# Kernel tuning notes

Measured on AMD Instinct MI355X. Metric: run time of the kernel, lower is better.

The kernel has to match this reference:

```python
import jax, jax.numpy as jnp
import numpy as np

HID = (128, 256, 128)  # nmp_qc NNet hidden layer sizes
D_IN = 256
TARGET = 256


def _mlp_params(key, n_in, n_out, prefix):
    sizes = (n_in,) + HID + (n_out,)
    params = {}
    for i in range(len(sizes) - 1):
        key, k1, k2 = jax.random.split(key, 3)
        fan_in = sizes[i]
        bound = 1.0 / np.sqrt(fan_in)
        params[f"{prefix}_W{i}"] = jax.random.uniform(k1, (sizes[i], sizes[i + 1]), jnp.float32, -bound, bound)
        params[f"{prefix}_b{i}"] = jax.random.uniform(k2, (sizes[i + 1],), jnp.float32, -bound, bound)
    return params, key


def _mlp(x, Ws, bs):
    # ReLU on all layers except the last (linear output), matching NNet
    for i in range(len(Ws) - 1):
        x = jax.nn.relu(x @ Ws[i] + bs[i])
    return x @ Ws[-1] + bs[-1]


def setup_inputs() -> dict:
    key = jax.random.key(0)
    k0, k1, key = jax.random.split(key, 3)
    B, N = 512, 256
    inp = {
        "h0": jax.random.normal(k0, (B, N, D_IN), jnp.float32),
        "hT": jax.random.normal(k1, (B, N, D_IN), jnp.float32),
    }
    gp, key = _mlp_params(key, 2 * D_IN, TARGET, "g")  # gate MLP: concat(h0,hT) -> target
    op, key = _mlp_params(key, D_IN, TARGET, "o")      # value MLP: hT -> target
    inp.update(gp)
    inp.update(op)
    return inp


def reference(h0, hT,
              g_W0, g_b0, g_W1, g_b1, g_W2, g_b2, g_W3, g_b3,
              o_W0, o_b0, o_W1, o_b1, o_W2, o_b2, o_W3, o_b3):
    gWs = (g_W0, g_W1, g_W2, g_W3)
    gbs = (g_b0, g_b1, g_b2, g_b3)
    oWs = (o_W0, o_W1, o_W2, o_W3)
    obs = (o_b0, o_b1, o_b2, o_b3)
    # gate: sigmoid(MLP1([h0; hT])) ; value: MLP2(hT)  -- all [B, N, target]
    gate = jax.nn.sigmoid(_mlp(jnp.concatenate([h0, hT], axis=-1), gWs, gbs))
    val = _mlp(hT, oWs, obs)
    # node validity mask: sum of initial features > 0, matching r_mpnn
    mask = (jnp.sum(h0, axis=-1, keepdims=True) > 0).astype(h0.dtype)  # [B, N, 1]
    return jnp.sum(mask * gate * val, axis=1)  # [B, target]
```

## Files before the change

kernel.cpp:

```cpp
#include <hip/hip_runtime.h>
#include <hip/hip_bf16.h>
#include <stdint.h>


typedef __attribute__((ext_vector_type(8))) short short8_t;
typedef __attribute__((ext_vector_type(16))) float f32x16;

#define ROWS 32
#define NWG  4096
#define NTHR 64

#define OFF_X 0
#define OFF_Y 8704
#define OFF_Z 17408
#define OFF_M 22016
#define LDS_TOTAL 22144

__device__ __forceinline__ short f2bf(float f) {
  union { float f; uint32_t u; } v; v.f = f;
  uint32_t r = (v.u + 0x7FFFu + ((v.u >> 16) & 1u)) >> 16;
  return (short)r;
}

template <int KT16, int KSTEPS, int CT>
__device__ __forceinline__ void gemmW(const short* actin, int Sin,
                                      const short* __restrict__ wsB, int ks0, int cb0,
                                      f32x16 (&acc)[CT], int lane) {
  const int n32 = lane & 31, q32 = lane >> 5;
#pragma unroll
  for (int ks = 0; ks < KSTEPS; ++ks) {
    const int kl = ks * 16 + q32 * 8;
    short8_t b[CT];
#pragma unroll
    for (int ct = 0; ct < CT; ++ct)
      b[ct] = *(const short8_t*)(wsB + (((cb0 + ct) * KT16 + ks0 + ks) << 9) + lane * 8);
    const short8_t a = *(const short8_t*)(actin + n32 * Sin + kl);
#pragma unroll
    for (int ct = 0; ct < CT; ++ct)
      acc[ct] = __builtin_amdgcn_mfma_f32_32x32x16_bf16(a, b[ct], acc[ct], 0, 0, 0);
  }
}

template <int CT, int ACTF>
__device__ __forceinline__ void epiW(f32x16 (&acc)[CT], short* actout, int Sout,
                                     const float* __restrict__ bias, int c0,
                                     int n32, int q32) {
#pragma unroll
  for (int ct = 0; ct < CT; ++ct) {
    const int c = c0 + ct * 32 + n32;
    const float bv = bias[c0 + ct * 32 + n32];
#pragma unroll
    for (int reg = 0; reg < 16; ++reg) {
      const int r = (reg & 3) + 8 * (reg >> 2) + 4 * q32;
      float v = acc[ct][reg] + bv;
      if (ACTF == 1) v = fmaxf(v, 0.f);
      actout[r * Sout + c] = f2bf(v);
    }
  }
}

template <bool MASKA>
__device__ __forceinline__ void stage_chunk(const float* __restrict__ src, int row0,
                                            int colbase, short* X, float* maskacc,
                                            int mmode, int lane) {
  const int c4 = lane & 31, rh = lane >> 5;
  float4 v[16];
#pragma unroll
  for (int it = 0; it < 16; ++it)
    v[it] = *(const float4*)(src + (size_t)(row0 + 2 * it + rh) * 256 + colbase + c4 * 4);
#pragma unroll
  for (int it = 0; it < 16; ++it) {
    const int r = 2 * it + rh;
    short4 pk; pk.x = f2bf(v[it].x); pk.y = f2bf(v[it].y); pk.z = f2bf(v[it].z); pk.w = f2bf(v[it].w);
    *(short4*)(X + r * 136 + c4 * 4) = pk;
    if (MASKA && mmode) {
      float s = v[it].x + v[it].y + v[it].z + v[it].w;
      s += __shfl_down(s, 16, 32);
      s += __shfl_down(s, 8, 32);
      s += __shfl_down(s, 4, 32);
      s += __shfl_down(s, 2, 32);
      s += __shfl_down(s, 1, 32);
      if (c4 == 0) {
        if (mmode == 1) maskacc[r] = s; else maskacc[r] += s;
      }
    }
  }
}

template <int NCH, bool MASKA>
__device__ __forceinline__ void streamW(const float* __restrict__ src0,
                                        const float* __restrict__ src1, int splitc,
                                        const short* __restrict__ wsB,
                                        const float* __restrict__ bias,
                                        short* X, short* Aout, float* maskacc,
                                        int row0, int lane) {
  constexpr int KT16 = NCH * 8;
  const int n32 = lane & 31, q32 = lane >> 5;
  f32x16 acc[4];
#pragma unroll
  for (int ct = 0; ct < 4; ++ct) acc[ct] = (f32x16)(0.f);
#pragma unroll
  for (int kc = 0; kc < NCH; ++kc) {
    const bool lo = (kc < splitc);
    const float* src = lo ? src0 : src1;
    const int colbase = (lo ? kc : kc - splitc) * 128;
    const int mm = MASKA ? (kc == 0 ? 1 : (lo ? 2 : 0)) : 0;
    stage_chunk<MASKA>(src, row0, colbase, X, maskacc, mm, lane);
    gemmW<KT16, 8, 4>(X, 136, wsB, kc * 8, 0, acc, lane);
  }
  epiW<4, 1>(acc, Aout, 136, bias, 0, n32, q32);
}

__device__ __forceinline__ void mid_pair(short* A, short* Z,
                                         const short* __restrict__ ws1,
                                         const float* __restrict__ b1,
                                         const short* __restrict__ ws2,
                                         const float* __restrict__ b2,
                                         int lane) {
  const int n32 = lane & 31, q32 = lane >> 5;
  f32x16 acc2[4];
#pragma unroll
  for (int ct = 0; ct < 4; ++ct) acc2[ct] = (f32x16)(0.f);
#pragma unroll
  for (int q = 0; q < 4; ++q) {
    f32x16 acc1[2];
    acc1[0] = (f32x16)(0.f); acc1[1] = (f32x16)(0.f);
    gemmW<8, 8, 2>(A, 136, ws1, 0, q * 2, acc1, lane);
    epiW<2, 1>(acc1, Z, 72, b1 + q * 64, 0, n32, q32);
    gemmW<16, 4, 4>(Z, 72, ws2, q * 4, 0, acc2, lane);
  }
  epiW<4, 1>(acc2, A, 136, b2, 0, n32, q32);
}

__device__ __forceinline__ void final_fuse(const short* Ag, const short* Av,
                                           const short* __restrict__ wsg,
                                           const float* __restrict__ bg,
                                           const short* __restrict__ wsv,
                                           const float* __restrict__ bv,
                                           const float* maskacc, float* __restrict__ out,
                                           int bidx, int lane) {
  const int n32 = lane & 31, q32 = lane >> 5;
#pragma unroll
  for (int q = 0; q < 4; ++q) {
    f32x16 ag[2]; ag[0] = (f32x16)(0.f); ag[1] = (f32x16)(0.f);
    gemmW<8, 8, 2>(Ag, 136, wsg, 0, q * 2, ag, lane);
    f32x16 av[2]; av[0] = (f32x16)(0.f); av[1] = (f32x16)(0.f);
    gemmW<8, 8, 2>(Av, 136, wsv, 0, q * 2, av, lane);
#pragma unroll
    for (int ct = 0; ct < 2; ++ct) {
      const int c = q * 64 + ct * 32 + n32;
      const float gb = bg[c], ob = bv[c];
      float s = 0.f;
#pragma unroll
      for (int reg = 0; reg < 16; ++reg) {
        const int r = (reg & 3) + 8 * (reg >> 2) + 4 * q32;
        if (maskacc[r] > 0.f) {
          const float g = 1.f / (1.f + __expf(-(ag[ct][reg] + gb)));
          s += g * (av[ct][reg] + ob);
        }
      }
      s += __shfl_down(s, 32);
      if (lane < 32) atomicAdd(out + bidx * 256 + c, s);
    }
  }
}

__global__ __launch_bounds__(NTHR, 2)
void readout_main(const float* __restrict__ h0, const float* __restrict__ hT,
                  const short* __restrict__ ws,
                  const float* __restrict__ gb0, const float* __restrict__ gb1,
                  const float* __restrict__ gb2, const float* __restrict__ gb3,
                  const float* __restrict__ ob0, const float* __restrict__ ob1,
                  const float* __restrict__ ob2, const float* __restrict__ ob3,
                  float* __restrict__ out) {
  __shared__ __align__(16) char smem[LDS_TOTAL];
  short* X = (short*)(smem + OFF_X);
  short* Y = (short*)(smem + OFF_Y);
  short* Z = (short*)(smem + OFF_Z);
  float* maskacc = (float*)(smem + OFF_M);

  const int lane = threadIdx.x;
  const int row0 = blockIdx.x * ROWS;
  const int bidx = row0 >> 8;

  streamW<4, true>(h0, hT, 2, ws + 0, gb0, X, Y, maskacc, row0, lane);
  mid_pair(Y, Z, ws + 65536, gb1, ws + 98304, gb2, lane);
  streamW<2, false>(hT, hT, 2, ws + 163840, ob0, X, X, maskacc, row0, lane);
  mid_pair(X, Z, ws + 196608, ob1, ws + 229376, ob2, lane);
  final_fuse(Y, X, ws + 131072, gb3, ws + 262144, ob3, maskacc, out, bidx, lane);
}

__global__ void prep(const float* __restrict__ W0, const float* __restrict__ W1,
                     const float* __restrict__ W2, const float* __restrict__ W3,
                     const float* __restrict__ W4, const float* __restrict__ W5,
                     const float* __restrict__ W6, const float* __restrict__ W7,
                     short* __restrict__ ws, float* __restrict__ out) {
  const int l = blockIdx.y;
  const int le = blockIdx.x * 256 + threadIdx.x;
  if (l == 1) { out[le] = 0.f; out[le + 65536] = 0.f; }
  int K, N, off; const float* W;
  switch (l) {
    case 0:  K = 512; N = 128; off = 0;      W = W0; break;
    case 1:  K = 128; N = 256; off = 65536;  W = W1; break;
    case 2:  K = 256; N = 128; off = 98304;  W = W2; break;
    case 3:  K = 128; N = 256; off = 131072; W = W3; break;
    case 4:  K = 256; N = 128; off = 163840; W = W4; break;
    case 5:  K = 128; N = 256; off = 196608; W = W5; break;
    case 6:  K = 256; N = 128; off = 229376; W = W6; break;
    default: K = 128; N = 256; off = 262144; W = W7; break;
  }
  if (le >= K * N) return;
  const int j = le & 7;
  const int lanei = (le >> 3) & 63;
  const int blk = le >> 9;
  const int kt16 = K >> 4;
  const int ks = blk % kt16, cb = blk / kt16;
  const int n = cb * 32 + (lanei & 31);
  const int k = ks * 16 + (lanei >> 5) * 8 + j;
  ws[off + le] = f2bf(W[k * N + n]);
}

extern "C" void kernel_launch(void* const* d_in, const int* in_sizes, int n_in,
                              void* d_out, int out_size, void* d_ws, size_t ws_size,
                              hipStream_t stream) {
  const float* h0  = (const float*)d_in[0];
  const float* hT  = (const float*)d_in[1];
  const float* gW0 = (const float*)d_in[2];  const float* gb0 = (const float*)d_in[3];
  const float* gW1 = (const float*)d_in[4];  const float* gb1 = (const float*)d_in[5];
  const float* gW2 = (const float*)d_in[6];  const float* gb2 = (const float*)d_in[7];
  const float* gW3 = (const float*)d_in[8];  const float* gb3 = (const float*)d_in[9];
  const float* oW0 = (const float*)d_in[10]; const float* ob0 = (const float*)d_in[11];
  const float* oW1 = (const float*)d_in[12]; const float* ob1 = (const float*)d_in[13];
  const float* oW2 = (const float*)d_in[14]; const float* ob2 = (const float*)d_in[15];
  const float* oW3 = (const float*)d_in[16]; const float* ob3 = (const float*)d_in[17];
  float* out = (float*)d_out;
  short* ws  = (short*)d_ws;

  prep<<<dim3(256, 8), 256, 0, stream>>>(gW0, gW1, gW2, gW3, oW0, oW1, oW2, oW3, ws, out);
  readout_main<<<NWG, NTHR, 0, stream>>>(h0, hT, ws,
                                         gb0, gb1, gb2, gb3,
                                         ob0, ob1, ob2, ob3, out);
}
```

Baseline: 523.9 us.

## Keep gate activations in registers to shrink LDS and raise occupancy

The gate branch's final hidden activations are now held in VGPRs as MFMA A-fragments rather than in a separate LDS buffer Y, so both branches reuse one activation buffer X. The LDS row stride is narrowed from 136 to 132, the staging loads are split into two batches of eight to reduce live registers, and launch bounds now request 3 waves per SIMD. The aim is more resident workgroups to hide global-load latency. The cost is 32 extra VGPRs held across the whole value branch, which may cause spills under the tighter register budget, and the new stride changes the LDS bank-conflict pattern.

```diff
diff --git a/kernel.cpp b/kernel.cpp
--- a/kernel.cpp
+++ b/kernel.cpp
@@ -10,11 +10,13 @@
 #define NWG  4096
 #define NTHR 64
 
+#define SA 132
+#define SZ 72
+
 #define OFF_X 0
-#define OFF_Y 8704
-#define OFF_Z 17408
-#define OFF_M 22016
-#define LDS_TOTAL 22144
+#define OFF_Z 8448
+#define OFF_M 13056
+#define LDS_TOTAL 13184
 
 __device__ __forceinline__ short f2bf(float f) {
   union { float f; uint32_t u; } v; v.f = f;
@@ -41,6 +43,22 @@
   }
 }
 
+template <int KT16, int CT>
+__device__ __forceinline__ void gemmRA(const short8_t (&aR)[8],
+                                       const short* __restrict__ wsB, int cb0,
+                                       f32x16 (&acc)[CT], int lane) {
+#pragma unroll
+  for (int ks = 0; ks < 8; ++ks) {
+    short8_t b[CT];
+#pragma unroll
+    for (int ct = 0; ct < CT; ++ct)
+      b[ct] = *(const short8_t*)(wsB + (((cb0 + ct) * KT16 + ks) << 9) + lane * 8);
+#pragma unroll
+    for (int ct = 0; ct < CT; ++ct)
+      acc[ct] = __builtin_amdgcn_mfma_f32_32x32x16_bf16(aR[ks], b[ct], acc[ct], 0, 0, 0);
+  }
+}
+
 template <int CT, int ACTF>
 __device__ __forceinline__ void epiW(f32x16 (&acc)[CT], short* actout, int Sout,
                                      const float* __restrict__ bias, int c0,
@@ -48,7 +66,7 @@
 #pragma unroll
   for (int ct = 0; ct < CT; ++ct) {
     const int c = c0 + ct * 32 + n32;
-    const float bv = bias[c0 + ct * 32 + n32];
+    const float bv = bias[c];
 #pragma unroll
     for (int reg = 0; reg < 16; ++reg) {
       const int r = (reg & 3) + 8 * (reg >> 2) + 4 * q32;
@@ -64,24 +82,27 @@
                                             int colbase, short* X, float* maskacc,
                                             int mmode, int lane) {
   const int c4 = lane & 31, rh = lane >> 5;
-  float4 v[16];
-#pragma unroll
-  for (int it = 0; it < 16; ++it)
-    v[it] = *(const float4*)(src + (size_t)(row0 + 2 * it + rh) * 256 + colbase + c4 * 4);
-#pragma unroll
-  for (int it = 0; it < 16; ++it) {
-    const int r = 2 * it + rh;
-    short4 pk; pk.x = f2bf(v[it].x); pk.y = f2bf(v[it].y); pk.z = f2bf(v[it].z); pk.w = f2bf(v[it].w);
-    *(short4*)(X + r * 136 + c4 * 4) = pk;
-    if (MASKA && mmode) {
-      float s = v[it].x + v[it].y + v[it].z + v[it].w;
-      s += __shfl_down(s, 16, 32);
-      s += __shfl_down(s, 8, 32);
-      s += __shfl_down(s, 4, 32);
-      s += __shfl_down(s, 2, 32);
-      s += __shfl_down(s, 1, 32);
-      if (c4 == 0) {
-        if (mmode == 1) maskacc[r] = s; else maskacc[r] += s;
+#pragma unroll
+  for (int g = 0; g < 2; ++g) {
+    float4 v[8];
+#pragma unroll
+    for (int it = 0; it < 8; ++it)
+      v[it] = *(const float4*)(src + (size_t)(row0 + g * 16 + 2 * it + rh) * 256 + colbase + c4 * 4);
+#pragma unroll
+    for (int it = 0; it < 8; ++it) {
+      const int r = g * 16 + 2 * it + rh;
+      short4 pk; pk.x = f2bf(v[it].x); pk.y = f2bf(v[it].y); pk.z = f2bf(v[it].z); pk.w = f2bf(v[it].w);
+      *(short4*)(X + r * SA + c4 * 4) = pk;
+      if (MASKA && mmode) {
+        float s = v[it].x + v[it].y + v[it].z + v[it].w;
+        s += __shfl_down(s, 16, 32);
+        s += __shfl_down(s, 8, 32);
+        s += __shfl_down(s, 4, 32);
+        s += __shfl_down(s, 2, 32);
+        s += __shfl_down(s, 1, 32);
+        if (c4 == 0) {
+          if (mmode == 1) maskacc[r] = s; else maskacc[r] += s;
+        }
       }
     }
   }
@@ -92,7 +113,7 @@
                                         const float* __restrict__ src1, int splitc,
                                         const short* __restrict__ wsB,
                                         const float* __restrict__ bias,
-                                        short* X, short* Aout, float* maskacc,
+                                        short* X, float* maskacc,
                                         int row0, int lane) {
   constexpr int KT16 = NCH * 8;
   const int n32 = lane & 31, q32 = lane >> 5;
@@ -106,9 +127,9 @@
     const int colbase = (lo ? kc : kc - splitc) * 128;
     const int mm = MASKA ? (kc == 0 ? 1 : (lo ? 2 : 0)) : 0;
     stage_chunk<MASKA>(src, row0, colbase, X, maskacc, mm, lane);
-    gemmW<KT16, 8, 4>(X, 136, wsB, kc * 8, 0, acc, lane);
-  }
-  epiW<4, 1>(acc, Aout, 136, bias, 0, n32, q32);
+    gemmW<KT16, 8, 4>(X, SA, wsB, kc * 8, 0, acc, lane);
+  }
+  epiW<4, 1>(acc, X, SA, bias, 0, n32, q32);
 }
 
 __device__ __forceinline__ void mid_pair(short* A, short* Z,
@@ -125,14 +146,14 @@
   for (int q = 0; q < 4; ++q) {
     f32x16 acc1[2];
     acc1[0] = (f32x16)(0.f); acc1[1] = (f32x16)(0.f);
-    gemmW<8, 8, 2>(A, 136, ws1, 0, q * 2, acc1, lane);
-    epiW<2, 1>(acc1, Z, 72, b1 + q * 64, 0, n32, q32);
-    gemmW<16, 4, 4>(Z, 72, ws2, q * 4, 0, acc2, lane);
-  }
-  epiW<4, 1>(acc2, A, 136, b2, 0, n32, q32);
-}
-
-__device__ __forceinline__ void final_fuse(const short* Ag, const short* Av,
+    gemmW<8, 8, 2>(A, SA, ws1, 0, q * 2, acc1, lane);
+    epiW<2, 1>(acc1, Z, SZ, b1 + q * 64, 0, n32, q32);
+    gemmW<16, 4, 4>(Z, SZ, ws2, q * 4, 0, acc2, lane);
+  }
+  epiW<4, 1>(acc2, A, SA, b2, 0, n32, q32);
+}
+
+__device__ __forceinline__ void final_fuse(const short8_t (&aG)[8], const short* Av,
                                            const short* __restrict__ wsg,
                                            const float* __restrict__ bg,
                                            const short* __restrict__ wsv,
@@ -143,9 +164,9 @@
 #pragma unroll
   for (int q = 0; q < 4; ++q) {
     f32x16 ag[2]; ag[0] = (f32x16)(0.f); ag[1] = (f32x16)(0.f);
-    gemmW<8, 8, 2>(Ag, 136, wsg, 0, q * 2, ag, lane);
+    gemmRA<8, 2>(aG, wsg, q * 2, ag, lane);
     f32x16 av[2]; av[0] = (f32x16)(0.f); av[1] = (f32x16)(0.f);
-    gemmW<8, 8, 2>(Av, 136, wsv, 0, q * 2, av, lane);
+    gemmW<8, 8, 2>(Av, SA, wsv, 0, q * 2, av, lane);
 #pragma unroll
     for (int ct = 0; ct < 2; ++ct) {
       const int c = q * 64 + ct * 32 + n32;
@@ -165,7 +186,7 @@
   }
 }
 
-__global__ __launch_bounds__(NTHR, 2)
+__global__ __launch_bounds__(NTHR, 3)
 void readout_main(const float* __restrict__ h0, const float* __restrict__ hT,
                   const short* __restrict__ ws,
                   const float* __restrict__ gb0, const float* __restrict__ gb1,
@@ -175,19 +196,23 @@
                   float* __restrict__ out) {
   __shared__ __align__(16) char smem[LDS_TOTAL];
   short* X = (short*)(smem + OFF_X);
-  short* Y = (short*)(smem + OFF_Y);
   short* Z = (short*)(smem + OFF_Z);
   float* maskacc = (float*)(smem + OFF_M);
 
   const int lane = threadIdx.x;
   const int row0 = blockIdx.x * ROWS;
   const int bidx = row0 >> 8;
-
-  streamW<4, true>(h0, hT, 2, ws + 0, gb0, X, Y, maskacc, row0, lane);
-  mid_pair(Y, Z, ws + 65536, gb1, ws + 98304, gb2, lane);
-  streamW<2, false>(hT, hT, 2, ws + 163840, ob0, X, X, maskacc, row0, lane);
+  const int n32 = lane & 31, q32 = lane >> 5;
+
+  streamW<4, true>(h0, hT, 2, ws + 0, gb0, X, maskacc, row0, lane);
+  mid_pair(X, Z, ws + 65536, gb1, ws + 98304, gb2, lane);
+  short8_t aG[8];
+#pragma unroll
+  for (int ks = 0; ks < 8; ++ks)
+    aG[ks] = *(const short8_t*)(X + n32 * SA + ks * 16 + q32 * 8);
+  streamW<2, false>(hT, hT, 2, ws + 163840, ob0, X, maskacc, row0, lane);
   mid_pair(X, Z, ws + 196608, ob1, ws + 229376, ob2, lane);
-  final_fuse(Y, X, ws + 131072, gb3, ws + 262144, ob3, maskacc, out, bidx, lane);
+  final_fuse(aG, X, ws + 131072, gb3, ws + 262144, ob3, maskacc, out, bidx, lane);
 }
 
 __global__ void prep(const float* __restrict__ W0, const float* __restrict__ W1,
```

After: 465.3 us. 11.2% less time.
